# Performance work log

Measured on AMD Instinct MI355X. Metric: run time of the kernel, lower is better.

## Reference

```python
import jax, jax.numpy as jnp
import numpy as np

D_MODEL = 512
N_STATE = 64
EMB_DIM = 512
LN_EPS = 1e-5


def setup_inputs() -> dict:
    key = jax.random.key(0)
    ks = jax.random.split(key, 12)
    B, L, d, N, e = 8, 2048, D_MODEL, N_STATE, EMB_DIM
    x = jax.random.normal(ks[0], (B, L, d), dtype=jnp.float32)
    emb = jax.random.normal(ks[1], (B, e), dtype=jnp.float32)
    # S4D kernel params
    A_real = -0.5 * jnp.ones((d, N), dtype=jnp.float32)
    A_imag = jnp.pi * jnp.broadcast_to(jnp.arange(N, dtype=jnp.float32)[None, :], (d, N))
    C = jax.random.normal(ks[2], (d, N, 2), dtype=jnp.float32) * 0.5
    dt_min, dt_max = 0.001, 0.1
    log_dt = jax.random.uniform(ks[3], (d,), dtype=jnp.float32) * (np.log(dt_max) - np.log(dt_min)) + np.log(dt_min)
    B_ssm = jnp.ones((d, N), dtype=jnp.float32)  # buffer, treated as constant
    # block params
    D_skip = jax.random.normal(ks[4], (d,), dtype=jnp.float32) * 0.01
    ln_gamma = jnp.ones((d,), dtype=jnp.float32)
    ln_beta = jnp.zeros((d,), dtype=jnp.float32)
    lim_out = 1.0 / np.sqrt(d)
    W_out = jax.random.uniform(ks[5], (2 * d, d), dtype=jnp.float32, minval=-lim_out, maxval=lim_out)
    b_out = jax.random.uniform(ks[6], (2 * d,), dtype=jnp.float32, minval=-lim_out, maxval=lim_out)
    lim_f = 1.0 / np.sqrt(e)
    W_film = jax.random.uniform(ks[7], (2 * d, e), dtype=jnp.float32, minval=-lim_f, maxval=lim_f)
    b_film = jax.random.uniform(ks[8], (2 * d,), dtype=jnp.float32, minval=-lim_f, maxval=lim_f)
    return dict(x=x, emb=emb, A_real=A_real, A_imag=A_imag, C=C, log_dt=log_dt,
                B_ssm=B_ssm, D_skip=D_skip, ln_gamma=ln_gamma, ln_beta=ln_beta,
                W_out=W_out, b_out=b_out, W_film=W_film, b_film=b_film)


def reference(x, emb, A_real, A_imag, C, log_dt, B_ssm, D_skip, ln_gamma, ln_beta,
              W_out, b_out, W_film, b_film):
    Bsz, L, d = x.shape
    residual = x
    # LayerNorm
    mu = jnp.mean(x, axis=-1, keepdims=True)
    var = jnp.mean((x - mu) ** 2, axis=-1, keepdims=True)
    xn = (x - mu) * jax.lax.rsqrt(var + LN_EPS) * ln_gamma + ln_beta
    # S4D kernel: K[d,l] = Re( sum_n (C*B)[d,n] * exp(dt*A)[d,n]**l ) * dt[d]
    dt = jnp.exp(log_dt)                                 # (d,)
    A = A_real + 1j * A_imag                             # (d,N)
    dtA = A * dt[:, None]                                # (d,N)
    Cc = (C[..., 0] + 1j * C[..., 1]) * B_ssm            # (d,N) complex
    l = jnp.arange(L, dtype=jnp.float32)
    powers = jnp.exp(dtA[:, :, None] * l)                # (d,N,L) complex, A_bar**l
    K = jnp.einsum('dn,dnl->dl', Cc, powers).real * dt[:, None]  # (d,L)
    # FFT convolution (circular over 2L -> linear)
    x_t = jnp.transpose(xn, (0, 2, 1))                   # (B,d,L)
    K_f = jnp.fft.rfft(K, n=2 * L)                       # (d,L+1)
    x_f = jnp.fft.rfft(x_t, n=2 * L)                     # (B,d,L+1)
    y = jnp.fft.irfft(K_f[None] * x_f, n=2 * L)[..., :L] # (B,d,L)
    y = y + x_t * D_skip[None, :, None]
    y = jnp.transpose(y, (0, 2, 1))                      # (B,L,d)
    # FiLM conditioning
    film = jax.nn.silu(emb) @ W_film.T + b_film          # (B,2d)
    scale, shift = jnp.split(film, 2, axis=-1)
    y = y * (1.0 + scale[:, None, :]) + shift[:, None, :]
    # out_proj: Linear(d,2d) + GLU
    proj = y @ W_out.T + b_out                           # (B,L,2d)
    a, g = jnp.split(proj, 2, axis=-1)
    y = a * jax.nn.sigmoid(g)
    return residual + y
```

## Files before the change

kernel.cpp:

```cpp
#include <hip/hip_runtime.h>
#include <math.h>

typedef __attribute__((ext_vector_type(8))) short bf8v;
typedef __attribute__((ext_vector_type(4))) float f4v;

union BF8 { bf8v v; unsigned short e[8]; };
union U4 { uint4 u; unsigned short e[8]; };

__device__ __forceinline__ float bf2f(unsigned short u) {
  union { unsigned int i; float f; } c; c.i = ((unsigned int)u) << 16; return c.f;
}
__device__ __forceinline__ unsigned short f2bf(float f) {
  union { float f; unsigned int i; } c; c.f = f;
  return (unsigned short)((c.i + 0x7fffu + ((c.i >> 16) & 1u)) >> 16);
}
__device__ __forceinline__ void gld16(const unsigned short* g, unsigned short* l) {
  __builtin_amdgcn_global_load_lds(
      (const __attribute__((address_space(1))) unsigned int*)g,
      (__attribute__((address_space(3))) unsigned int*)l, 16, 0, 0);
}

__global__ __launch_bounds__(256) void prelude_kernel(
    const float* __restrict__ emb, const float* __restrict__ Wf,
    const float* __restrict__ bfm, float* __restrict__ film,
    const float* __restrict__ W, unsigned short* __restrict__ Wb,
    const float* __restrict__ A_real, const float* __restrict__ A_imag,
    const float* __restrict__ Cc, const float* __restrict__ log_dt,
    const float* __restrict__ B_ssm, const float* __restrict__ D_skip,
    unsigned short* __restrict__ Pre, unsigned short* __restrict__ Pim,
    unsigned short* __restrict__ Mre, unsigned short* __restrict__ Mim,
    unsigned short* __restrict__ Tt, float* __restrict__ W64r, float* __restrict__ W64i,
    const float* __restrict__ x, const float* __restrict__ gamma,
    const float* __restrict__ beta, unsigned short* __restrict__ xT) {
  __shared__ __align__(16) char sh[16 * 520 * 2];
  const int blk = blockIdx.x;
  const int tid = threadIdx.x;
  if (blk < 2048) {
    const int gw = blk * 4 + (tid >> 6);
    const int lane = tid & 63;
    const int b = gw >> 10, j = gw & 1023;
    const float4* ep = (const float4*)(emb + (size_t)b * 512) + lane * 2;
    const float4* wp = (const float4*)(Wf + (size_t)j * 512) + lane * 2;
    float acc = 0.f;
    #pragma unroll
    for (int i = 0; i < 2; i++) {
      const float4 e = ep[i], w = wp[i];
      acc += (e.x / (1.f + __expf(-e.x))) * w.x;
      acc += (e.y / (1.f + __expf(-e.y))) * w.y;
      acc += (e.z / (1.f + __expf(-e.z))) * w.z;
      acc += (e.w / (1.f + __expf(-e.w))) * w.w;
    }
    #pragma unroll
    for (int off = 32; off >= 1; off >>= 1) acc += __shfl_xor(acc, off);
    if (lane == 0) film[(size_t)b * 1024 + j] = acc + bfm[j];
  } else if (blk < 2560) {
    const int i = (blk - 2048) * 256 + tid;
    const float4 v = ((const float4*)W)[i];
    uint2 pk;
    pk.x = (unsigned)f2bf(v.x) | ((unsigned)f2bf(v.y) << 16);
    pk.y = (unsigned)f2bf(v.z) | ((unsigned)f2bf(v.w) << 16);
    ((uint2*)Wb)[i] = pk;
  } else if (blk < 3072) {
    float* Ktl = (float*)sh;
    const int d = blk - 2560;
    const float dt = __expf(log_dt[d]);
    const int wv = tid >> 6, n = tid & 63;
    {
      const int dn = d * 64 + n;
      const float ar = dt * A_real[dn], ai = dt * A_imag[dn];
      const float bs = B_ssm[dn] * dt;
      const float c0 = Cc[dn * 2] * bs, c1 = Cc[dn * 2 + 1] * bs;
      #pragma unroll
      for (int i = 0; i < 16; i++) {
        const float tau = (float)(wv * 16 + i);
        const float ex = __expf(ar * tau);
        float sn, cs; __sincosf(ai * tau, &sn, &cs);
        float r = ex * (c0 * cs - c1 * sn);
        #pragma unroll
        for (int off = 32; off >= 1; off >>= 1) r += __shfl_xor(r, off);
        if (n == 0) Ktl[wv * 16 + i] = (wv * 16 + i == 0) ? (r + D_skip[d]) : r;
      }
    }
    __syncthreads();
    for (int g = tid; g < 512; g += 256) {
      const int nn = g >> 3, s0 = (g & 7) * 8;
      const int dn = d * 64 + nn;
      const float ar = dt * A_real[dn], ai = dt * A_imag[dn];
      union { unsigned short s[8]; uint4 u; } pr, pi;
      #pragma unroll
      for (int j = 0; j < 8; j++) {
        const float k = (float)(63 - (s0 + j));
        const float ex = __expf(ar * k);
        float sn, cs; __sincosf(ai * k, &sn, &cs);
        pr.s[j] = f2bf(ex * cs); pi.s[j] = f2bf(ex * sn);
      }
      *(uint4*)(Pre + (size_t)d * 4096 + nn * 64 + s0) = pr.u;
      *(uint4*)(Pim + (size_t)d * 4096 + nn * 64 + s0) = pi.u;
    }
    for (int g = tid; g < 512; g += 256) {
      const int t = g >> 3, n0 = (g & 7) * 8;
      union { unsigned short s[8]; uint4 u; } mr, mi;
      #pragma unroll
      for (int j = 0; j < 8; j++) {
        const int dn = d * 64 + n0 + j;
        const float ar = dt * A_real[dn], ai = dt * A_imag[dn];
        const float bs = B_ssm[dn] * dt;
        const float c0 = Cc[dn * 2] * bs, c1 = Cc[dn * 2 + 1] * bs;
        const float k = (float)(t + 1);
        const float ex = __expf(ar * k);
        float sn, cs; __sincosf(ai * k, &sn, &cs);
        mr.s[j] = f2bf(ex * (c0 * cs - c1 * sn));
        mi.s[j] = f2bf(-ex * (c0 * sn + c1 * cs));
      }
      *(uint4*)(Mre + (size_t)d * 4096 + t * 64 + n0) = mr.u;
      *(uint4*)(Mim + (size_t)d * 4096 + t * 64 + n0) = mi.u;
    }
    for (int g = tid; g < 512; g += 256) {
      const int t = g >> 3, s0 = (g & 7) * 8;
      union { unsigned short s[8]; uint4 u; } tv;
      #pragma unroll
      for (int j = 0; j < 8; j++) {
        const int s = s0 + j;
        tv.s[j] = (s <= t) ? f2bf(Ktl[t - s]) : (unsigned short)0;
      }
      *(uint4*)(Tt + (size_t)d * 4096 + t * 64 + s0) = tv.u;
    }
    if (tid < 64) {
      const int dn = d * 64 + tid;
      const float ex = __expf(dt * A_real[dn] * 64.f);
      float sn, cs; __sincosf(dt * A_imag[dn] * 64.f, &sn, &cs);
      W64r[d * 64 + tid] = ex * cs;
      W64i[d * 64 + tid] = ex * sn;
    }
  } else {
    unsigned short* t = (unsigned short*)sh;
    const int r0 = (blk - 3072) * 16;
    const int wv = tid >> 6, lane = tid & 63;
    const float4* gp = (const float4*)gamma + lane * 2;
    const float4* bp = (const float4*)beta  + lane * 2;
    const float4 g0 = gp[0], g1 = gp[1], bb0 = bp[0], bb1 = bp[1];
    #pragma unroll
    for (int i = 0; i < 4; i++) {
      const int r = wv * 4 + i;
      const float4* xr = (const float4*)(x + (size_t)(r0 + r) * 512) + lane * 2;
      const float4 v0 = xr[0], v1 = xr[1];
      float s  = v0.x + v0.y + v0.z + v0.w + v1.x + v1.y + v1.z + v1.w;
      float sq = v0.x*v0.x + v0.y*v0.y + v0.z*v0.z + v0.w*v0.w
               + v1.x*v1.x + v1.y*v1.y + v1.z*v1.z + v1.w*v1.w;
      #pragma unroll
      for (int off = 32; off >= 1; off >>= 1) {
        s  += __shfl_xor(s, off);
        sq += __shfl_xor(sq, off);
      }
      const float mu   = s * (1.f / 512.f);
      const float var  = sq * (1.f / 512.f) - mu * mu;
      const float rstd = rsqrtf(var + 1e-5f);
      uint4 pk;
      pk.x = (unsigned)f2bf((v0.x - mu) * rstd * g0.x + bb0.x)
           | ((unsigned)f2bf((v0.y - mu) * rstd * g0.y + bb0.y) << 16);
      pk.y = (unsigned)f2bf((v0.z - mu) * rstd * g0.z + bb0.z)
           | ((unsigned)f2bf((v0.w - mu) * rstd * g0.w + bb0.w) << 16);
      pk.z = (unsigned)f2bf((v1.x - mu) * rstd * g1.x + bb1.x)
           | ((unsigned)f2bf((v1.y - mu) * rstd * g1.y + bb1.y) << 16);
      pk.w = (unsigned)f2bf((v1.z - mu) * rstd * g1.z + bb1.z)
           | ((unsigned)f2bf((v1.w - mu) * rstd * g1.w + bb1.w) << 16);
      *(uint4*)&t[r * 520 + lane * 8] = pk;
    }
    __syncthreads();
    const int p = tid;
    union { unsigned short s[8]; uint4 u; } a0, a1, b0, b1;
    #pragma unroll
    for (int r = 0; r < 8; r++) {
      const unsigned v = *(const unsigned*)&t[r * 520 + p * 2];
      a0.s[r] = (unsigned short)(v & 0xffffu);
      b0.s[r] = (unsigned short)(v >> 16);
    }
    #pragma unroll
    for (int r = 0; r < 8; r++) {
      const unsigned v = *(const unsigned*)&t[(r + 8) * 520 + p * 2];
      a1.s[r] = (unsigned short)(v & 0xffffu);
      b1.s[r] = (unsigned short)(v >> 16);
    }
    unsigned short* o0 = xT + (size_t)(2 * p) * 16384 + r0;
    *(uint4*)o0 = a0.u; *(uint4*)(o0 + 8) = a1.u;
    unsigned short* o1 = xT + (size_t)(2 * p + 1) * 16384 + r0;
    *(uint4*)o1 = b0.u; *(uint4*)(o1 + 8) = b1.u;
  }
}

__global__ __launch_bounds__(256, 2) void ssm_kernel(
    const unsigned short* __restrict__ xT,
    const unsigned short* __restrict__ Pre, const unsigned short* __restrict__ Pim,
    const unsigned short* __restrict__ Mre, const unsigned short* __restrict__ Mim,
    const unsigned short* __restrict__ Tt,
    const float* __restrict__ W64r, const float* __restrict__ W64i,
    const float* __restrict__ film, unsigned short* __restrict__ y2) {
  extern __shared__ char smem[];
  unsigned short* Pr = (unsigned short*)smem;
  unsigned short* Pi = Pr + 64 * 68;
  unsigned short* Mr = Pi + 64 * 68;
  unsigned short* Mi = Mr + 64 * 68;
  unsigned short* Tl = Mi + 64 * 68;
  unsigned int*   Eb = (unsigned int*)(Tl + 64 * 68);

  const int d = blockIdx.x;
  const int tid = threadIdx.x;
  const int wv = tid >> 6, lane = tid & 63;
  const int n15 = lane & 15, quad = lane >> 4;
  const int j0 = wv * 32;
  const size_t dtab = (size_t)d * 4096;

  {
    const unsigned short* gt[5] = {Pre + dtab, Pim + dtab, Mre + dtab, Mim + dtab, Tt + dtab};
    unsigned short* lt[5] = {Pr, Pi, Mr, Mi, Tl};
    #pragma unroll
    for (int i = 0; i < 10; i++) {
      const int idx = tid + i * 256;
      const int tb = idx >> 9, r = (idx >> 3) & 63, g = idx & 7;
      const uint4 v = *(const uint4*)(gt[tb] + r * 64 + g * 8);
      *(uint4*)&lt[tb][r * 68 + g * 8] = v;
    }
  }
  bf8v Xf[2][2][2];
  #pragma unroll
  for (int h = 0; h < 2; h++)
    #pragma unroll
    for (int ct = 0; ct < 2; ct++)
      #pragma unroll
      for (int kq = 0; kq < 2; kq++)
        Xf[h][ct][kq] = *(const bf8v*)(xT + (size_t)d * 16384 +
            (h * 128 + j0 + ct * 16 + n15) * 64 + kq * 32 + quad * 8);
  __syncthreads();

  #pragma unroll
  for (int h = 0; h < 2; h++) {
    const int jg0 = h * 128;
    {
      f4v Er[4][2], Ei[4][2];
      #pragma unroll
      for (int a = 0; a < 4; a++)
        #pragma unroll
        for (int b2 = 0; b2 < 2; b2++) { Er[a][b2] = (f4v){0,0,0,0}; Ei[a][b2] = (f4v){0,0,0,0}; }
      #pragma unroll
      for (int mt = 0; mt < 4; mt++)
        #pragma unroll
        for (int kq = 0; kq < 2; kq++) {
          const bf8v pr = *(const bf8v*)&Pr[(mt * 16 + n15) * 68 + kq * 32 + quad * 8];
          const bf8v pi = *(const bf8v*)&Pi[(mt * 16 + n15) * 68 + kq * 32 + quad * 8];
          #pragma unroll
          for (int ct = 0; ct < 2; ct++) {
            Er[mt][ct] = __builtin_amdgcn_mfma_f32_16x16x32_bf16(pr, Xf[h][ct][kq], Er[mt][ct], 0, 0, 0);
            Ei[mt][ct] = __builtin_amdgcn_mfma_f32_16x16x32_bf16(pi, Xf[h][ct][kq], Ei[mt][ct], 0, 0, 0);
          }
        }
      #pragma unroll
      for (int mt = 0; mt < 4; mt++)
        #pragma unroll
        for (int ct = 0; ct < 2; ct++)
          #pragma unroll
          for (int i = 0; i < 4; i++) {
            const int row = mt * 16 + quad * 4 + i;
            const int col = j0 + ct * 16 + n15;
            Eb[row * 131 + col] =
                (unsigned)f2bf(Er[mt][ct][i]) | ((unsigned)f2bf(Ei[mt][ct][i]) << 16);
          }
    }
    __syncthreads();

    {
      const int n = lane, bp = wv;
      const float wre = W64r[d * 64 + n], wim = W64i[d * 64 + n];
      unsigned int* row = &Eb[n * 131 + bp * 32];
      float str = 0.f, sti = 0.f;
      #pragma unroll
      for (int c = 0; c < 32; c++) {
        const unsigned u = row[c];
        row[c] = (unsigned)f2bf(str) | ((unsigned)f2bf(sti) << 16);
        const float er = bf2f((unsigned short)(u & 0xffffu));
        const float ei = bf2f((unsigned short)(u >> 16));
        const float nr = er + wre * str - wim * sti;
        const float ni = ei + wre * sti + wim * str;
        str = nr; sti = ni;
      }
    }
    __syncthreads();

    f4v Y[4][2];
    #pragma unroll
    for (int a = 0; a < 4; a++)
      #pragma unroll
      for (int b2 = 0; b2 < 2; b2++) Y[a][b2] = (f4v){0,0,0,0};

    #pragma unroll
    for (int mt = 0; mt < 4; mt++)
      #pragma unroll
      for (int kq = 0; kq < 2; kq++) {
        const bf8v tf = *(const bf8v*)&Tl[(mt * 16 + n15) * 68 + kq * 32 + quad * 8];
        #pragma unroll
        for (int ct = 0; ct < 2; ct++)
          Y[mt][ct] = __builtin_amdgcn_mfma_f32_16x16x32_bf16(tf, Xf[h][ct][kq], Y[mt][ct], 0, 0, 0);
      }

    #pragma unroll
    for (int kq = 0; kq < 2; kq++) {
      BF8 ir[2], ii[2];
      #pragma unroll
      for (int ct = 0; ct < 2; ct++)
        #pragma unroll
        for (int jj = 0; jj < 8; jj++) {
          const unsigned u = Eb[(kq * 32 + quad * 8 + jj) * 131 + (j0 + ct * 16 + n15)];
          ir[ct].e[jj] = (unsigned short)(u & 0xffffu);
          ii[ct].e[jj] = (unsigned short)(u >> 16);
        }
      #pragma unroll
      for (int mt = 0; mt < 4; mt++) {
        const bf8v mr = *(const bf8v*)&Mr[(mt * 16 + n15) * 68 + kq * 32 + quad * 8];
        const bf8v mi = *(const bf8v*)&Mi[(mt * 16 + n15) * 68 + kq * 32 + quad * 8];
        #pragma unroll
        for (int ct = 0; ct < 2; ct++) {
          Y[mt][ct] = __builtin_amdgcn_mfma_f32_16x16x32_bf16(mr, ir[ct].v, Y[mt][ct], 0, 0, 0);
          Y[mt][ct] = __builtin_amdgcn_mfma_f32_16x16x32_bf16(mi, ii[ct].v, Y[mt][ct], 0, 0, 0);
        }
      }
    }

    #pragma unroll
    for (int ct = 0; ct < 2; ct++) {
      const int jglob = jg0 + j0 + ct * 16 + n15;
      const int b = jglob >> 5;
      const float scl = 1.f + film[b * 1024 + d];
      const float shf = film[b * 1024 + 512 + d];
      #pragma unroll
      for (int mt = 0; mt < 4; mt++) {
        union { unsigned short s[4]; uint2 u; } pk;
        #pragma unroll
        for (int i = 0; i < 4; i++)
          pk.s[i] = f2bf(fmaf(Y[mt][ct][i], scl, shf));
        *(uint2*)(y2 + (size_t)d * 16384 + jglob * 64 + mt * 16 + quad * 4) = pk.u;
      }
    }
    if (h == 0) __syncthreads();
  }
}

__global__ __launch_bounds__(256, 3) void gemm_kernel(
    const unsigned short* __restrict__ y2, const unsigned short* __restrict__ Wb,
    const float* __restrict__ bo, const float* __restrict__ x,
    float* __restrict__ out) {
  __shared__ __align__(16) unsigned short Al[128 * 64];
  __shared__ __align__(16) unsigned short Bl[128 * 64];
  const int m0 = blockIdx.x * 128, cp0 = blockIdx.y * 64;
  const int tid = threadIdx.x;
  const int wv = tid >> 6, lane = tid & 63;
  const int n15 = lane & 15, quad = lane >> 4;
  const int lr = lane >> 3;
  const int lg = lane & 7;
  const int sg = (lg ^ lr) * 8;
  const int mg = tid & 15;
  const int kg = tid >> 4;

  f4v acc[2][8];
  #pragma unroll
  for (int mi = 0; mi < 2; mi++)
    #pragma unroll
    for (int t4 = 0; t4 < 8; t4++) acc[mi][t4] = (f4v){0.f, 0.f, 0.f, 0.f};

  for (int kk = 0; kk < 8; kk++) {
    U4 q[4];
    #pragma unroll
    for (int r = 0; r < 4; r++)
      q[r].u = *(const uint4*)(y2 + (size_t)(kk * 64 + kg * 4 + r) * 16384 + m0 + mg * 8);
    #pragma unroll
    for (int i = 0; i < 4; i++) {
      const int row = wv * 32 + i * 8 + lr;
      const int cg = (row < 64) ? (cp0 + row) : (512 + cp0 + row - 64);
      gld16(Wb + (size_t)cg * 512 + kk * 64 + sg, Bl + (wv * 32 + i * 8) * 64);
    }
    #pragma unroll
    for (int i = 0; i < 8; i++) {
      const int m = mg * 8 + i;
      union { unsigned short e[4]; uint2 u; } o;
      o.e[0] = q[0].e[i]; o.e[1] = q[1].e[i]; o.e[2] = q[2].e[i]; o.e[3] = q[3].e[i];
      *(uint2*)&Al[m * 64 + (((kg >> 1) ^ i ^ (mg & 7)) & 7) * 8 + (kg & 1) * 4] = o.u;
    }
    __syncthreads();
    #pragma unroll
    for (int kq = 0; kq < 2; kq++) {
      bf8v av[2], bv[8];
      #pragma unroll
      for (int mt = 0; mt < 2; mt++) {
        const int row = wv * 32 + mt * 16 + n15;
        const int g = kq * 4 + quad;
        av[mt] = *(const bf8v*)&Al[row * 64 + (((g ^ (row & 7) ^ ((row >> 3) & 7)) & 7) * 8)];
      }
      #pragma unroll
      for (int t4 = 0; t4 < 8; t4++) {
        const int row = t4 * 16 + n15;
        bv[t4] = *(const bf8v*)&Bl[row * 64 + (((kq * 4 + quad) ^ (row & 7)) * 8)];
      }
      #pragma unroll
      for (int mt = 0; mt < 2; mt++)
        #pragma unroll
        for (int t4 = 0; t4 < 8; t4++)
          acc[mt][t4] = __builtin_amdgcn_mfma_f32_16x16x32_bf16(av[mt], bv[t4], acc[mt][t4], 0, 0, 0);
    }
    __syncthreads();
  }
  #pragma unroll
  for (int mt = 0; mt < 2; mt++) {
    const int mrow = m0 + wv * 32 + mt * 16 + quad * 4;
    #pragma unroll
    for (int t4 = 0; t4 < 4; t4++) {
      const int c = cp0 + t4 * 16 + n15;
      const float ba = bo[c], bg = bo[512 + c];
      #pragma unroll
      for (int i = 0; i < 4; i++) {
        const size_t off = (size_t)(mrow + i) * 512 + c;
        const float av2 = acc[mt][t4][i] + ba;
        const float gv = acc[mt][t4 + 4][i] + bg;
        out[off] = x[off] + av2 * (1.f / (1.f + __expf(-gv)));
      }
    }
  }
}

extern "C" void kernel_launch(void* const* d_in, const int* in_sizes, int n_in,
                              void* d_out, int out_size, void* d_ws, size_t ws_size,
                              hipStream_t stream) {
  const float* x      = (const float*)d_in[0];
  const float* emb    = (const float*)d_in[1];
  const float* A_real = (const float*)d_in[2];
  const float* A_imag = (const float*)d_in[3];
  const float* C      = (const float*)d_in[4];
  const float* log_dt = (const float*)d_in[5];
  const float* B_ssm  = (const float*)d_in[6];
  const float* D_skip = (const float*)d_in[7];
  const float* gamma  = (const float*)d_in[8];
  const float* beta   = (const float*)d_in[9];
  const float* W_out  = (const float*)d_in[10];
  const float* b_out  = (const float*)d_in[11];
  const float* W_film = (const float*)d_in[12];
  const float* b_film = (const float*)d_in[13];
  float* out = (float*)d_out;

  char* ws = (char*)d_ws;
  size_t o = 0;
  float*          film = (float*)(ws + o);          o += 32768;
  unsigned short* xT   = (unsigned short*)(ws + o); o += 16777216;
  unsigned short* Wb   = (unsigned short*)(ws + o); o += 1048576;
  unsigned short* Pre  = (unsigned short*)(ws + o); o += 4194304;
  unsigned short* Pim  = (unsigned short*)(ws + o); o += 4194304;
  unsigned short* Mre  = (unsigned short*)(ws + o); o += 4194304;
  unsigned short* Mim  = (unsigned short*)(ws + o); o += 4194304;
  unsigned short* Tt   = (unsigned short*)(ws + o); o += 4194304;
  float*          W64r = (float*)(ws + o);          o += 131072;
  float*          W64i = (float*)(ws + o);          o += 131072;
  unsigned short* y2   = (unsigned short*)(ws + o); o += 16777216;

  prelude_kernel<<<dim3(4096), dim3(256), 0, stream>>>(
      emb, W_film, b_film, film, W_out, Wb,
      A_real, A_imag, C, log_dt, B_ssm, D_skip,
      Pre, Pim, Mre, Mim, Tt, W64r, W64i,
      x, gamma, beta, xT);
  ssm_kernel<<<dim3(512), dim3(256), 77056, stream>>>(xT, Pre, Pim, Mre, Mim, Tt,
                                                      W64r, W64i, film, y2);
  gemm_kernel<<<dim3(128, 8), dim3(256), 0, stream>>>(y2, Wb, b_out, x, out);
}
```

Baseline: 184.5 us.

## Compute S4D tables directly into shared memory inside the SSM kernel

The per-channel S4D tables (the powers P, the modes M, the Toeplitz block T and the 64-step transition W64) were built by the prelude, written to global memory and reloaded by the SSM kernel. They are now computed inside the SSM kernel straight into LDS, which removes about 20 MB of global writes and reads and shrinks the prelude grid. The GEMM launch is also changed to a 1D grid with a remapped block index. The cost is extra transcendental work in each SSM block before its main loop starts.

```diff
diff --git a/kernel.cpp b/kernel.cpp
--- a/kernel.cpp
+++ b/kernel.cpp
@@ -24,15 +24,9 @@
     const float* __restrict__ emb, const float* __restrict__ Wf,
     const float* __restrict__ bfm, float* __restrict__ film,
     const float* __restrict__ W, unsigned short* __restrict__ Wb,
-    const float* __restrict__ A_real, const float* __restrict__ A_imag,
-    const float* __restrict__ Cc, const float* __restrict__ log_dt,
-    const float* __restrict__ B_ssm, const float* __restrict__ D_skip,
-    unsigned short* __restrict__ Pre, unsigned short* __restrict__ Pim,
-    unsigned short* __restrict__ Mre, unsigned short* __restrict__ Mim,
-    unsigned short* __restrict__ Tt, float* __restrict__ W64r, float* __restrict__ W64i,
     const float* __restrict__ x, const float* __restrict__ gamma,
     const float* __restrict__ beta, unsigned short* __restrict__ xT) {
-  __shared__ __align__(16) char sh[16 * 520 * 2];
+  __shared__ __align__(16) unsigned short t[16 * 520];
   const int blk = blockIdx.x;
   const int tid = threadIdx.x;
   if (blk < 2048) {
@@ -60,81 +54,8 @@
     pk.x = (unsigned)f2bf(v.x) | ((unsigned)f2bf(v.y) << 16);
     pk.y = (unsigned)f2bf(v.z) | ((unsigned)f2bf(v.w) << 16);
     ((uint2*)Wb)[i] = pk;
-  } else if (blk < 3072) {
-    float* Ktl = (float*)sh;
-    const int d = blk - 2560;
-    const float dt = __expf(log_dt[d]);
-    const int wv = tid >> 6, n = tid & 63;
-    {
-      const int dn = d * 64 + n;
-      const float ar = dt * A_real[dn], ai = dt * A_imag[dn];
-      const float bs = B_ssm[dn] * dt;
-      const float c0 = Cc[dn * 2] * bs, c1 = Cc[dn * 2 + 1] * bs;
-      #pragma unroll
-      for (int i = 0; i < 16; i++) {
-        const float tau = (float)(wv * 16 + i);
-        const float ex = __expf(ar * tau);
-        float sn, cs; __sincosf(ai * tau, &sn, &cs);
-        float r = ex * (c0 * cs - c1 * sn);
-        #pragma unroll
-        for (int off = 32; off >= 1; off >>= 1) r += __shfl_xor(r, off);
-        if (n == 0) Ktl[wv * 16 + i] = (wv * 16 + i == 0) ? (r + D_skip[d]) : r;
-      }
-    }
-    __syncthreads();
-    for (int g = tid; g < 512; g += 256) {
-      const int nn = g >> 3, s0 = (g & 7) * 8;
-      const int dn = d * 64 + nn;
-      const float ar = dt * A_real[dn], ai = dt * A_imag[dn];
-      union { unsigned short s[8]; uint4 u; } pr, pi;
-      #pragma unroll
-      for (int j = 0; j < 8; j++) {
-        const float k = (float)(63 - (s0 + j));
-        const float ex = __expf(ar * k);
-        float sn, cs; __sincosf(ai * k, &sn, &cs);
-        pr.s[j] = f2bf(ex * cs); pi.s[j] = f2bf(ex * sn);
-      }
-      *(uint4*)(Pre + (size_t)d * 4096 + nn * 64 + s0) = pr.u;
-      *(uint4*)(Pim + (size_t)d * 4096 + nn * 64 + s0) = pi.u;
-    }
-    for (int g = tid; g < 512; g += 256) {
-      const int t = g >> 3, n0 = (g & 7) * 8;
-      union { unsigned short s[8]; uint4 u; } mr, mi;
-      #pragma unroll
-      for (int j = 0; j < 8; j++) {
-        const int dn = d * 64 + n0 + j;
-        const float ar = dt * A_real[dn], ai = dt * A_imag[dn];
-        const float bs = B_ssm[dn] * dt;
-        const float c0 = Cc[dn * 2] * bs, c1 = Cc[dn * 2 + 1] * bs;
-        const float k = (float)(t + 1);
-        const float ex = __expf(ar * k);
-        float sn, cs; __sincosf(ai * k, &sn, &cs);
-        mr.s[j] = f2bf(ex * (c0 * cs - c1 * sn));
-        mi.s[j] = f2bf(-ex * (c0 * sn + c1 * cs));
-      }
-      *(uint4*)(Mre + (size_t)d * 4096 + t * 64 + n0) = mr.u;
-      *(uint4*)(Mim + (size_t)d * 4096 + t * 64 + n0) = mi.u;
-    }
-    for (int g = tid; g < 512; g += 256) {
-      const int t = g >> 3, s0 = (g & 7) * 8;
-      union { unsigned short s[8]; uint4 u; } tv;
-      #pragma unroll
-      for (int j = 0; j < 8; j++) {
-        const int s = s0 + j;
-        tv.s[j] = (s <= t) ? f2bf(Ktl[t - s]) : (unsigned short)0;
-      }
-      *(uint4*)(Tt + (size_t)d * 4096 + t * 64 + s0) = tv.u;
-    }
-    if (tid < 64) {
-      const int dn = d * 64 + tid;
-      const float ex = __expf(dt * A_real[dn] * 64.f);
-      float sn, cs; __sincosf(dt * A_imag[dn] * 64.f, &sn, &cs);
-      W64r[d * 64 + tid] = ex * cs;
-      W64i[d * 64 + tid] = ex * sn;
-    }
   } else {
-    unsigned short* t = (unsigned short*)sh;
-    const int r0 = (blk - 3072) * 16;
+    const int r0 = (blk - 2560) * 16;
     const int wv = tid >> 6, lane = tid & 63;
     const float4* gp = (const float4*)gamma + lane * 2;
     const float4* bp = (const float4*)beta  + lane * 2;
@@ -190,10 +111,9 @@
 
 __global__ __launch_bounds__(256, 2) void ssm_kernel(
     const unsigned short* __restrict__ xT,
-    const unsigned short* __restrict__ Pre, const unsigned short* __restrict__ Pim,
-    const unsigned short* __restrict__ Mre, const unsigned short* __restrict__ Mim,
-    const unsigned short* __restrict__ Tt,
-    const float* __restrict__ W64r, const float* __restrict__ W64i,
+    const float* __restrict__ A_real, const float* __restrict__ A_imag,
+    const float* __restrict__ Cc, const float* __restrict__ log_dt,
+    const float* __restrict__ B_ssm, const float* __restrict__ D_skip,
     const float* __restrict__ film, unsigned short* __restrict__ y2) {
   extern __shared__ char smem[];
   unsigned short* Pr = (unsigned short*)smem;
@@ -208,19 +128,7 @@
   const int wv = tid >> 6, lane = tid & 63;
   const int n15 = lane & 15, quad = lane >> 4;
   const int j0 = wv * 32;
-  const size_t dtab = (size_t)d * 4096;
-
-  {
-    const unsigned short* gt[5] = {Pre + dtab, Pim + dtab, Mre + dtab, Mim + dtab, Tt + dtab};
-    unsigned short* lt[5] = {Pr, Pi, Mr, Mi, Tl};
-    #pragma unroll
-    for (int i = 0; i < 10; i++) {
-      const int idx = tid + i * 256;
-      const int tb = idx >> 9, r = (idx >> 3) & 63, g = idx & 7;
-      const uint4 v = *(const uint4*)(gt[tb] + r * 64 + g * 8);
-      *(uint4*)&lt[tb][r * 68 + g * 8] = v;
-    }
-  }
+
   bf8v Xf[2][2][2];
   #pragma unroll
   for (int h = 0; h < 2; h++)
@@ -230,6 +138,79 @@
       for (int kq = 0; kq < 2; kq++)
         Xf[h][ct][kq] = *(const bf8v*)(xT + (size_t)d * 16384 +
             (h * 128 + j0 + ct * 16 + n15) * 64 + kq * 32 + quad * 8);
+
+  const float dt = __expf(log_dt[d]);
+  float w64re, w64im;
+  {
+    const int dn = d * 64 + lane;
+    const float ex = __expf(dt * A_real[dn] * 64.f);
+    float sn, cs; __sincosf(dt * A_imag[dn] * 64.f, &sn, &cs);
+    w64re = ex * cs; w64im = ex * sn;
+  }
+  {
+    float* Ktl = (float*)Eb;
+    const int dn = d * 64 + lane;
+    const float ar = dt * A_real[dn], ai = dt * A_imag[dn];
+    const float bs = B_ssm[dn] * dt;
+    const float c0 = Cc[dn * 2] * bs, c1 = Cc[dn * 2 + 1] * bs;
+    #pragma unroll
+    for (int i = 0; i < 16; i++) {
+      const float tau = (float)(wv * 16 + i);
+      const float ex = __expf(ar * tau);
+      float sn, cs; __sincosf(ai * tau, &sn, &cs);
+      float r = ex * (c0 * cs - c1 * sn);
+      #pragma unroll
+      for (int off = 32; off >= 1; off >>= 1) r += __shfl_xor(r, off);
+      if (lane == 0) Ktl[wv * 16 + i] = (wv * 16 + i == 0) ? (r + D_skip[d]) : r;
+    }
+  }
+  __syncthreads();
+  for (int g = tid; g < 512; g += 256) {
+    const int nn = g >> 3, s0 = (g & 7) * 8;
+    const int dn = d * 64 + nn;
+    const float ar = dt * A_real[dn], ai = dt * A_imag[dn];
+    union { unsigned short s[8]; uint4 u; } pr, pi;
+    #pragma unroll
+    for (int j = 0; j < 8; j++) {
+      const float k = (float)(63 - (s0 + j));
+      const float ex = __expf(ar * k);
+      float sn, cs; __sincosf(ai * k, &sn, &cs);
+      pr.s[j] = f2bf(ex * cs); pi.s[j] = f2bf(ex * sn);
+    }
+    *(uint4*)&Pr[nn * 68 + s0] = pr.u;
+    *(uint4*)&Pi[nn * 68 + s0] = pi.u;
+  }
+  for (int g = tid; g < 512; g += 256) {
+    const int t = g >> 3, n0 = (g & 7) * 8;
+    union { unsigned short s[8]; uint4 u; } mr, mi;
+    #pragma unroll
+    for (int j = 0; j < 8; j++) {
+      const int dn = d * 64 + n0 + j;
+      const float ar = dt * A_real[dn], ai = dt * A_imag[dn];
+      const float bs = B_ssm[dn] * dt;
+      const float c0 = Cc[dn * 2] * bs, c1 = Cc[dn * 2 + 1] * bs;
+      const float k = (float)(t + 1);
+      const float ex = __expf(ar * k);
+      float sn, cs; __sincosf(ai * k, &sn, &cs);
+      mr.s[j] = f2bf(ex * (c0 * cs - c1 * sn));
+      mi.s[j] = f2bf(-ex * (c0 * sn + c1 * cs));
+    }
+    *(uint4*)&Mr[t * 68 + n0] = mr.u;
+    *(uint4*)&Mi[t * 68 + n0] = mi.u;
+  }
+  {
+    const float* Ktl = (const float*)Eb;
+    for (int g = tid; g < 512; g += 256) {
+      const int t = g >> 3, s0 = (g & 7) * 8;
+      union { unsigned short s[8]; uint4 u; } tv;
+      #pragma unroll
+      for (int j = 0; j < 8; j++) {
+        const int s = s0 + j;
+        tv.s[j] = (s <= t) ? f2bf(Ktl[t - s]) : (unsigned short)0;
+      }
+      *(uint4*)&Tl[t * 68 + s0] = tv.u;
+    }
+  }
   __syncthreads();
 
   #pragma unroll
@@ -268,9 +249,7 @@
     __syncthreads();
 
     {
-      const int n = lane, bp = wv;
-      const float wre = W64r[d * 64 + n], wim = W64i[d * 64 + n];
-      unsigned int* row = &Eb[n * 131 + bp * 32];
+      unsigned int* row = &Eb[lane * 131 + wv * 32];
       float str = 0.f, sti = 0.f;
       #pragma unroll
       for (int c = 0; c < 32; c++) {
@@ -278,8 +257,8 @@
         row[c] = (unsigned)f2bf(str) | ((unsigned)f2bf(sti) << 16);
         const float er = bf2f((unsigned short)(u & 0xffffu));
         const float ei = bf2f((unsigned short)(u >> 16));
-        const float nr = er + wre * str - wim * sti;
-        const float ni = ei + wre * sti + wim * str;
+        const float nr = er + w64re * str - w64im * sti;
+        const float ni = ei + w64re * sti + w64im * str;
         str = nr; sti = ni;
       }
     }
@@ -349,7 +328,7 @@
     float* __restrict__ out) {
   __shared__ __align__(16) unsigned short Al[128 * 64];
   __shared__ __align__(16) unsigned short Bl[128 * 64];
-  const int m0 = blockIdx.x * 128, cp0 = blockIdx.y * 64;
+  const int m0 = (blockIdx.x & 127) * 128, cp0 = (blockIdx.x >> 7) * 64;
   const int tid = threadIdx.x;
   const int wv = tid >> 6, lane = tid & 63;
   const int n15 = lane & 15, quad = lane >> 4;
@@ -448,21 +427,11 @@
   float*          film = (float*)(ws + o);          o += 32768;
   unsigned short* xT   = (unsigned short*)(ws + o); o += 16777216;
   unsigned short* Wb   = (unsigned short*)(ws + o); o += 1048576;
-  unsigned short* Pre  = (unsigned short*)(ws + o); o += 4194304;
-  unsigned short* Pim  = (unsigned short*)(ws + o); o += 4194304;
-  unsigned short* Mre  = (unsigned short*)(ws + o); o += 4194304;
-  unsigned short* Mim  = (unsigned short*)(ws + o); o += 4194304;
-  unsigned short* Tt   = (unsigned short*)(ws + o); o += 4194304;
-  float*          W64r = (float*)(ws + o);          o += 131072;
-  float*          W64i = (float*)(ws + o);          o += 131072;
   unsigned short* y2   = (unsigned short*)(ws + o); o += 16777216;
 
-  prelude_kernel<<<dim3(4096), dim3(256), 0, stream>>>(
-      emb, W_film, b_film, film, W_out, Wb,
-      A_real, A_imag, C, log_dt, B_ssm, D_skip,
-      Pre, Pim, Mre, Mim, Tt, W64r, W64i,
-      x, gamma, beta, xT);
-  ssm_kernel<<<dim3(512), dim3(256), 77056, stream>>>(xT, Pre, Pim, Mre, Mim, Tt,
-                                                      W64r, W64i, film, y2);
-  gemm_kernel<<<dim3(128, 8), dim3(256), 0, stream>>>(y2, Wb, b_out, x, out);
-}
+  prelude_kernel<<<dim3(3584), dim3(256), 0, stream>>>(
+      emb, W_film, b_film, film, W_out, Wb, x, gamma, beta, xT);
+  ssm_kernel<<<dim3(512), dim3(256), 77056, stream>>>(
+      xT, A_real, A_imag, C, log_dt, B_ssm, D_skip, film, y2);
+  gemm_kernel<<<dim3(1024), dim3(256), 0, stream>>>(y2, Wb, b_out, x, out);
+}
```

New measurement: 184.9 us. No clear change (+0.2%).
